# Performance work log

Hardware: AMD Instinct MI355X
Metric: run time of the kernel (lower is better)

The kernel has to match this reference:

```python
import jax, jax.numpy as jnp
import numpy as np

B, T, D, H1, H2, O = 64, 256, 512, 1024, 1024, 512


def setup_inputs() -> dict:
    key = jax.random.key(0)
    ks = jax.random.split(key, 6)
    s = 0.05  # weight scale for numerical sanity
    return {
        "x": jax.random.normal(ks[0], (B, T, D), dtype=jnp.float32),
        "W1": jax.random.normal(ks[1], (D, 4 * H1), dtype=jnp.float32) * s,
        "U1": jax.random.normal(ks[2], (H1, 4 * H1), dtype=jnp.float32) * s,
        "b1": jnp.zeros((4 * H1,), dtype=jnp.float32),
        "W2": jax.random.normal(ks[3], (H1, 4 * H2), dtype=jnp.float32) * s,
        "U2": jax.random.normal(ks[4], (H2, 4 * H2), dtype=jnp.float32) * s,
        "b2": jnp.zeros((4 * H2,), dtype=jnp.float32),
        "Wd": jax.random.normal(ks[5], (H2, O), dtype=jnp.float32) * s,
        "bd": jnp.zeros((O,), dtype=jnp.float32),
    }


def _lstm_layer(x_seq, W, U, b, units):
    """Run an LSTM layer over x_seq [B,T,Din]; returns full h sequence [B,T,units].

    Keras LSTMCell gate order: i, f, c(g), o; sigmoid recurrent activation, tanh activation.
    """
    # Precompute input projections for all timesteps: [T, B, 4*units]
    xz = (jnp.einsum('btd,dk->tbk', x_seq, W) + b).astype(x_seq.dtype)
    bsz = x_seq.shape[0]
    h0 = jnp.zeros((bsz, units), dtype=x_seq.dtype)
    c0 = jnp.zeros((bsz, units), dtype=x_seq.dtype)

    def step(carry, xz_t):
        h, c = carry
        z = xz_t + h @ U
        zi, zf, zg, zo = jnp.split(z, 4, axis=-1)
        c_new = jax.nn.sigmoid(zf) * c + jax.nn.sigmoid(zi) * jnp.tanh(zg)
        h_new = jax.nn.sigmoid(zo) * jnp.tanh(c_new)
        return (h_new, c_new), h_new

    (_, _), hs = jax.lax.scan(step, (h0, c0), xz)  # hs: [T, B, units]
    return jnp.transpose(hs, (1, 0, 2))


def reference(x, W1, U1, b1, W2, U2, b2, Wd, bd):
    seq1 = _lstm_layer(x, W1, U1, b1, H1)          # [B, T, H1]
    seq2 = _lstm_layer(seq1, W2, U2, b2, H2)       # [B, T, H2]
    h_last = seq2[:, -1, :]                        # final hidden state of layer 2
    return h_last @ Wd + bd
```

## Files before the change

### kernel.cpp

```cpp
#include <hip/hip_runtime.h>


typedef __bf16 bf16x8 __attribute__((ext_vector_type(8)));
typedef float f32x4 __attribute__((ext_vector_type(4)));
typedef unsigned int u32x4 __attribute__((ext_vector_type(4)));
typedef unsigned short u16;

#define LDS_Z_OFF 131584
#define LDS_TOTAL 148992

__device__ __forceinline__ u16 f2bf(float f) {
  unsigned u = __float_as_uint(f);
  unsigned r = (u + 0x7FFFu + ((u >> 16) & 1u)) >> 16;
  return (u16)r;
}

__global__ __launch_bounds__(256) void transpose_to_bf16(
    const float* __restrict__ in, u16* __restrict__ out, int R, int C) {
  __shared__ float tile[32][33];
  int tx = threadIdx.x & 31, ty = threadIdx.x >> 5;
  int c0 = blockIdx.x * 32, r0 = blockIdx.y * 32;
#pragma unroll
  for (int i = 0; i < 4; ++i)
    tile[ty + i * 8][tx] = in[(size_t)(r0 + ty + i * 8) * C + (c0 + tx)];
  __syncthreads();
#pragma unroll
  for (int i = 0; i < 4; ++i)
    out[(size_t)(c0 + ty + i * 8) * R + (r0 + tx)] = f2bf(tile[tx][ty + i * 8]);
}

__global__ __launch_bounds__(256) void convert_to_bf16(
    const float* __restrict__ in, u16* __restrict__ out, int n4) {
  int i = blockIdx.x * 256 + threadIdx.x;
  if (i >= n4) return;
  float4 v = reinterpret_cast<const float4*>(in)[i];
  ushort4 o;
  o.x = f2bf(v.x); o.y = f2bf(v.y); o.z = f2bf(v.z); o.w = f2bf(v.w);
  reinterpret_cast<ushort4*>(out)[i] = o;
}

__global__ void init_bar(unsigned* __restrict__ bar) { bar[threadIdx.x] = 0u; }

__device__ __forceinline__ void store_h_sc1(u16* p, unsigned v) {
  asm volatile("global_store_short %0, %1, off sc1" :: "v"(p), "v"(v) : "memory");
}

template <int I, int C0, int DEPTH, bool SC0, bool SC1>
__device__ __forceinline__ void stg_issue(u32x4 (&ring)[DEPTH],
    const u16* b0, const u16* b1) {
  constexpr int OFF = (I < C0 ? I : I - C0) * 256;
  if constexpr (I < C0) {
    if constexpr (SC0)
      asm volatile("global_load_dwordx4 %0, %1, off offset:%2 sc1"
                   : "=v"(ring[I % DEPTH]) : "v"(b0), "i"(OFF));
    else
      asm volatile("global_load_dwordx4 %0, %1, off offset:%2"
                   : "=v"(ring[I % DEPTH]) : "v"(b0), "i"(OFF));
  } else {
    if constexpr (SC1)
      asm volatile("global_load_dwordx4 %0, %1, off offset:%2 sc1"
                   : "=v"(ring[I % DEPTH]) : "v"(b1), "i"(OFF));
    else
      asm volatile("global_load_dwordx4 %0, %1, off offset:%2"
                   : "=v"(ring[I % DEPTH]) : "v"(b1), "i"(OFF));
  }
}

template <int I, int NPRE, int C0, int DEPTH, bool SC0, bool SC1>
__device__ __forceinline__ void stg_pre(u32x4 (&ring)[DEPTH],
    const u16* b0, const u16* b1) {
  if constexpr (I < NPRE) {
    stg_issue<I, C0, DEPTH, SC0, SC1>(ring, b0, b1);
    stg_pre<I + 1, NPRE, C0, DEPTH, SC0, SC1>(ring, b0, b1);
  }
}

template <int I, int NC, int C0, int DEPTH, bool SC0, bool SC1>
__device__ __forceinline__ void stg_main(u32x4 (&ring)[DEPTH],
    const u16* b0, const u16* b1, u16* lrow) {
  if constexpr (I < NC) {
    constexpr int ISSUED = (I + DEPTH < NC) ? I + DEPTH : NC;
    constexpr int WAIT = ISSUED - I - 1;
    asm volatile("s_waitcnt vmcnt(%1)" : "+v"(ring[I % DEPTH]) : "i"(WAIT));
    *(u32x4*)(lrow + I * 128) = ring[I % DEPTH];
    if constexpr (I + DEPTH < NC)
      stg_issue<I + DEPTH, C0, DEPTH, SC0, SC1>(ring, b0, b1);
    stg_main<I + 1, NC, C0, DEPTH, SC0, SC1>(ring, b0, b1, lrow);
  }
}

template <int NC, int C0, bool SC0, bool SC1>
__device__ __forceinline__ void stage(const u16* b0, const u16* b1, u16* lrow) {
  u32x4 ring[8];
  stg_pre<0, (NC < 8 ? NC : 8), C0, 8, SC0, SC1>(ring, b0, b1);
  stg_main<0, NC, C0, 8, SC0, SC1>(ring, b0, b1, lrow);
}

__device__ __forceinline__ void grid_barrier(unsigned* __restrict__ bar,
                                             int g, unsigned want) {
  asm volatile("s_waitcnt vmcnt(0)" ::: "memory");
  __syncthreads();
  if (threadIdx.x == 0) {
    unsigned old = __hip_atomic_fetch_add(bar + 32 * (1 + g), 1u,
                                          __ATOMIC_RELAXED, __HIP_MEMORY_SCOPE_AGENT);
    if (old == 32u * want - 1u) {
      unsigned r = __hip_atomic_fetch_add(bar, 1u, __ATOMIC_RELAXED,
                                          __HIP_MEMORY_SCOPE_AGENT);
      if (r == 8u * want - 1u) {
#pragma unroll
        for (int i = 0; i < 8; ++i)
          __hip_atomic_store(bar + 32 * (9 + i), want, __ATOMIC_RELAXED,
                             __HIP_MEMORY_SCOPE_AGENT);
      }
    }
    while (__hip_atomic_load(bar + 32 * (9 + g), __ATOMIC_RELAXED,
                             __HIP_MEMORY_SCOPE_AGENT) < want)
      __builtin_amdgcn_s_sleep(1);
  }
  __syncthreads();
}

template <int NC, int C0, bool SC0, bool IS2>
__device__ __forceinline__ void run_layer(
    const u16* __restrict__ xbf, const u16* __restrict__ Wt,
    const u16* __restrict__ Ut, const float* __restrict__ bias,
    u16* __restrict__ h1r, u16* __restrict__ h2r, unsigned* __restrict__ bar,
    int strip, int mhalf, char* smem, int g) {
  constexpr int KE = NC * 128;
  constexpr int P = KE + 8;
  constexpr int WCH = C0 * 4;
  u16* Alds = (u16*)smem;
  float* Zlds = (float*)(smem + LDS_Z_OFF);
  const int tid = threadIdx.x;
  const int wave = tid >> 6, lane = tid & 63;
  const int cp = wave & 1, kq = wave >> 1;
  const int quad = lane >> 4, l16 = lane & 15;

  bf16x8 breg[2][NC];
#pragma unroll
  for (int gi = 0; gi < 2; ++gi) {
    const int col = (2 * cp + gi) * 1024 + strip * 16 + l16;
#pragma unroll
    for (int j = 0; j < NC; ++j) {
      const int ks = kq * NC + j;
      breg[gi][j] = (ks < WCH)
        ? *(const bf16x8*)(Wt + (size_t)col * (C0 * 128) + ks * 32 + quad * 8)
        : *(const bf16x8*)(Ut + (size_t)col * 1024 + (ks - WCH) * 32 + quad * 8);
    }
  }

  const int eu = tid & 15, em = tid >> 4;
  const float bz0 = bias[strip * 16 + eu];
  const float bz1 = bias[1024 + strip * 16 + eu];
  const float bz2 = bias[2048 + strip * 16 + eu];
  const float bz3 = bias[3072 + strip * 16 + eu];
  float c = 0.f;

  const int sr = tid >> 4, l8 = tid & 15;
  const int sb = mhalf * 32 + sr;
  u16* lrow = Alds + sr * P + l8 * 8;

  const u16* a0p = Alds + l16 * P + quad * 8 + kq * (NC * 32);
  const u16* a1p = a0p + 16 * P;

  const int zc0 = cp * 32 + l16, zc1 = zc0 + 16;
  float* zb = Zlds + (kq & 1) * (32 * 68);

  for (int s = 0; s <= 256; ++s) {
    const int t = IS2 ? (s - 1) : s;
    if (t >= 0 && t < 256) {
      const u16 *b0, *b1;
      if constexpr (IS2) {
        b0 = h1r + (size_t)(t & 1) * 65536 + (size_t)sb * 1024 + l8 * 8;
        b1 = h2r + (size_t)((t - 1) & 1) * 65536 + (size_t)sb * 1024 + l8 * 8;
      } else {
        b0 = xbf + ((size_t)sb * 256 + t) * 512 + l8 * 8;
        b1 = h1r + (size_t)((t - 1) & 1) * 65536 + (size_t)sb * 1024 + l8 * 8;
      }
      if (t > 0) {
        stage<NC, C0, SC0, true>(b0, b1, lrow);
      } else {
        stage<C0, C0, SC0, true>(b0, b0, lrow);
#pragma unroll
        for (int i = C0; i < NC; ++i)
          *(u32x4*)(lrow + i * 128) = (u32x4){0u, 0u, 0u, 0u};
      }
      __syncthreads();

      f32x4 acc00 = {0.f, 0.f, 0.f, 0.f}, acc10 = {0.f, 0.f, 0.f, 0.f};
      f32x4 acc01 = {0.f, 0.f, 0.f, 0.f}, acc11 = {0.f, 0.f, 0.f, 0.f};
#pragma unroll
      for (int j = 0; j < NC; ++j) {
        bf16x8 a0 = *(const bf16x8*)(a0p + j * 32);
        bf16x8 a1 = *(const bf16x8*)(a1p + j * 32);
        acc00 = __builtin_amdgcn_mfma_f32_16x16x32_bf16(a0, breg[0][j], acc00, 0, 0, 0);
        acc10 = __builtin_amdgcn_mfma_f32_16x16x32_bf16(a1, breg[0][j], acc10, 0, 0, 0);
        acc01 = __builtin_amdgcn_mfma_f32_16x16x32_bf16(a0, breg[1][j], acc01, 0, 0, 0);
        acc11 = __builtin_amdgcn_mfma_f32_16x16x32_bf16(a1, breg[1][j], acc11, 0, 0, 0);
      }

      if (kq < 2) {
#pragma unroll
        for (int i = 0; i < 4; ++i) {
          zb[(quad * 4 + i) * 68 + zc0] = acc00[i];
          zb[(16 + quad * 4 + i) * 68 + zc0] = acc10[i];
          zb[(quad * 4 + i) * 68 + zc1] = acc01[i];
          zb[(16 + quad * 4 + i) * 68 + zc1] = acc11[i];
        }
      }
      __syncthreads();
      if (kq >= 2) {
#pragma unroll
        for (int i = 0; i < 4; ++i) {
          zb[(quad * 4 + i) * 68 + zc0] += acc00[i];
          zb[(16 + quad * 4 + i) * 68 + zc0] += acc10[i];
          zb[(quad * 4 + i) * 68 + zc1] += acc01[i];
          zb[(16 + quad * 4 + i) * 68 + zc1] += acc11[i];
        }
      }
      __syncthreads();

      u16* hring = IS2 ? h2r : h1r;
      u16* hp = hring + (size_t)(t & 1) * 65536 +
                (size_t)(mhalf * 32 + em) * 1024 + strip * 16 + eu;
      {
        float zi = Zlds[em * 68 + eu]      + Zlds[(32 + em) * 68 + eu]      + bz0;
        float zf = Zlds[em * 68 + 16 + eu] + Zlds[(32 + em) * 68 + 16 + eu] + bz1;
        float zg = Zlds[em * 68 + 32 + eu] + Zlds[(32 + em) * 68 + 32 + eu] + bz2;
        float zo = Zlds[em * 68 + 48 + eu] + Zlds[(32 + em) * 68 + 48 + eu] + bz3;
        float ig = 1.f / (1.f + __expf(-zi));
        float fg = 1.f / (1.f + __expf(-zf));
        float gg = 1.f - 2.f / (1.f + __expf(2.f * zg));
        float og = 1.f / (1.f + __expf(-zo));
        c = fg * c + ig * gg;
        float h = og * (1.f - 2.f / (1.f + __expf(2.f * c)));
        store_h_sc1(hp, (unsigned)f2bf(h));
      }
    }
    if (s < 256) grid_barrier(bar, g, (unsigned)(s + 1));
  }
}

__global__ __launch_bounds__(512, 2) void lstm_persistent(
    const u16* __restrict__ xbf,
    const u16* __restrict__ W1t,
    const u16* __restrict__ U1t,
    const float* __restrict__ b1,
    const u16* __restrict__ W2t,
    const u16* __restrict__ U2t,
    const float* __restrict__ b2,
    u16* __restrict__ h1r,
    u16* __restrict__ h2r,
    unsigned* __restrict__ bar) {
  extern __shared__ __align__(16) char smem[];
  const int blk = blockIdx.x;
  const bool is2 = blk >= 128;
  const int lb = is2 ? blk - 128 : blk;
  const int strip = lb >> 1;
  const int mhalf = lb & 1;
  const int g = blk & 7;
  if (!is2)
    run_layer<12, 4, false, false>(xbf, W1t, U1t, b1, h1r, h2r, bar,
                                   strip, mhalf, smem, g);
  else
    run_layer<16, 8, true, true>(xbf, W2t, U2t, b2, h1r, h2r, bar,
                                 strip, mhalf, smem, g);
}

__global__ __launch_bounds__(64) void dense_kernel(
    const u16* __restrict__ h2,
    const u16* __restrict__ Wdt,
    const float* __restrict__ bd,
    float* __restrict__ out) {
  int mt = blockIdx.x >> 5;
  int nt = blockIdx.x & 31;
  int lane = threadIdx.x;
  int quad = lane >> 4, l16 = lane & 15;
  f32x4 acc = {0.f, 0.f, 0.f, 0.f};
  const u16* ap = h2 + (size_t)(mt * 16 + l16) * 1024 + quad * 8;
  const u16* bp = Wdt + (size_t)(nt * 16 + l16) * 1024 + quad * 8;
#pragma unroll
  for (int ks = 0; ks < 32; ++ks) {
    bf16x8 a = *reinterpret_cast<const bf16x8*>(ap + ks * 32);
    bf16x8 b = *reinterpret_cast<const bf16x8*>(bp + ks * 32);
    acc = __builtin_amdgcn_mfma_f32_16x16x32_bf16(a, b, acc, 0, 0, 0);
  }
  int colo = nt * 16 + l16;
  float bias = bd[colo];
#pragma unroll
  for (int i = 0; i < 4; ++i)
    out[(size_t)(mt * 16 + quad * 4 + i) * 512 + colo] = acc[i] + bias;
}

extern "C" void kernel_launch(void* const* d_in, const int* in_sizes, int n_in,
                              void* d_out, int out_size, void* d_ws, size_t ws_size,
                              hipStream_t stream) {
  const float* x  = (const float*)d_in[0];
  const float* W1 = (const float*)d_in[1];
  const float* U1 = (const float*)d_in[2];
  const float* b1 = (const float*)d_in[3];
  const float* W2 = (const float*)d_in[4];
  const float* U2 = (const float*)d_in[5];
  const float* b2 = (const float*)d_in[6];
  const float* Wd = (const float*)d_in[7];
  const float* bd = (const float*)d_in[8];
  float* out = (float*)d_out;

  char* p = (char*)d_ws;
  auto carve = [&](size_t bytes) -> char* {
    char* r = p;
    p += (bytes + 255) & ~(size_t)255;
    return r;
  };
  u16* W1t = (u16*)carve((size_t)4096 * 512 * 2);
  u16* U1t = (u16*)carve((size_t)4096 * 1024 * 2);
  u16* W2t = (u16*)carve((size_t)4096 * 1024 * 2);
  u16* U2t = (u16*)carve((size_t)4096 * 1024 * 2);
  u16* Wdt = (u16*)carve((size_t)512 * 1024 * 2);
  u16* xbf = (u16*)carve((size_t)64 * 256 * 512 * 2);
  u16* h1r = (u16*)carve((size_t)2 * 64 * 1024 * 2);
  u16* h2r = (u16*)carve((size_t)2 * 64 * 1024 * 2);
  unsigned* bar = (unsigned*)carve(1024 * 4);
  (void)ws_size; (void)in_sizes; (void)n_in; (void)out_size;

  transpose_to_bf16<<<dim3(128, 16), 256, 0, stream>>>(W1, W1t, 512, 4096);
  transpose_to_bf16<<<dim3(128, 32), 256, 0, stream>>>(U1, U1t, 1024, 4096);
  transpose_to_bf16<<<dim3(128, 32), 256, 0, stream>>>(W2, W2t, 1024, 4096);
  transpose_to_bf16<<<dim3(128, 32), 256, 0, stream>>>(U2, U2t, 1024, 4096);
  transpose_to_bf16<<<dim3(16, 32), 256, 0, stream>>>(Wd, Wdt, 1024, 512);
  convert_to_bf16<<<8192, 256, 0, stream>>>(x, xbf, 64 * 256 * 512 / 4);
  init_bar<<<1, 1024, 0, stream>>>(bar);

  hipFuncSetAttribute(reinterpret_cast<const void*>(lstm_persistent),
                      hipFuncAttributeMaxDynamicSharedMemorySize, LDS_TOTAL);
  lstm_persistent<<<256, 512, LDS_TOTAL, stream>>>(
      xbf, W1t, U1t, b1, W2t, U2t, b2, h1r, h2r, bar);

  dense_kernel<<<128, 64, 0, stream>>>(h2r + 65536, Wdt, bd, out);
}
```

Baseline: 1.468 ms.

## Decouple LSTM layers with per-layer barriers and epoch flags over an 8-deep h1 ring

Replaces the single grid-wide barrier that locked both layers into one step with a separate 128-block barrier per layer. Layer 1 publishes an epoch counter after each step, and layer 2 polls it before consuming h1. Layer 1 in turn waits on layer 2's epoch so it never runs more than 8 steps ahead, and h1 moves to an 8-slot ring. This lets the layers drift relative to each other and shrinks each barrier, at the cost of extra polling and a larger h1 buffer.

```diff
diff --git a/kernel.cpp b/kernel.cpp
--- a/kernel.cpp
+++ b/kernel.cpp
@@ -39,7 +39,9 @@
   reinterpret_cast<ushort4*>(out)[i] = o;
 }
 
-__global__ void init_bar(unsigned* __restrict__ bar) { bar[threadIdx.x] = 0u; }
+__global__ void init_bar(unsigned* __restrict__ bar) {
+  bar[blockIdx.x * 1024 + threadIdx.x] = 0u;
+}
 
 __device__ __forceinline__ void store_h_sc1(u16* p, unsigned v) {
   asm volatile("global_store_short %0, %1, off sc1" :: "v"(p), "v"(v) : "memory");
@@ -96,26 +98,40 @@
   stg_main<0, NC, C0, 8, SC0, SC1>(ring, b0, b1, lrow);
 }
 
-__device__ __forceinline__ void grid_barrier(unsigned* __restrict__ bar,
-                                             int g, unsigned want) {
+__device__ __forceinline__ void group_barrier(unsigned* __restrict__ ubar,
+                                              unsigned* __restrict__ epub,
+                                              int g, unsigned want) {
   asm volatile("s_waitcnt vmcnt(0)" ::: "memory");
   __syncthreads();
   if (threadIdx.x == 0) {
-    unsigned old = __hip_atomic_fetch_add(bar + 32 * (1 + g), 1u,
+    unsigned old = __hip_atomic_fetch_add(ubar + 32 * (1 + g), 1u,
                                           __ATOMIC_RELAXED, __HIP_MEMORY_SCOPE_AGENT);
     if (old == 32u * want - 1u) {
-      unsigned r = __hip_atomic_fetch_add(bar, 1u, __ATOMIC_RELAXED,
+      unsigned r = __hip_atomic_fetch_add(ubar, 1u, __ATOMIC_RELAXED,
                                           __HIP_MEMORY_SCOPE_AGENT);
-      if (r == 8u * want - 1u) {
-#pragma unroll
-        for (int i = 0; i < 8; ++i)
-          __hip_atomic_store(bar + 32 * (9 + i), want, __ATOMIC_RELAXED,
+      if (r == 4u * want - 1u) {
+        __hip_atomic_store(epub, want, __ATOMIC_RELAXED,
+                           __HIP_MEMORY_SCOPE_AGENT);
+#pragma unroll
+        for (int i = 0; i < 4; ++i)
+          __hip_atomic_store(ubar + 32 * (9 + i), want, __ATOMIC_RELAXED,
                              __HIP_MEMORY_SCOPE_AGENT);
       }
     }
-    while (__hip_atomic_load(bar + 32 * (9 + g), __ATOMIC_RELAXED,
+    while (__hip_atomic_load(ubar + 32 * (9 + g), __ATOMIC_RELAXED,
                              __HIP_MEMORY_SCOPE_AGENT) < want)
       __builtin_amdgcn_s_sleep(1);
+  }
+  __syncthreads();
+}
+
+__device__ __forceinline__ void wait_epoch(unsigned* __restrict__ p,
+                                           unsigned v, unsigned& seen) {
+  if (threadIdx.x == 0) {
+    while (seen < v) {
+      seen = __hip_atomic_load(p, __ATOMIC_RELAXED, __HIP_MEMORY_SCOPE_AGENT);
+      if (seen < v) __builtin_amdgcn_s_sleep(2);
+    }
   }
   __syncthreads();
 }
@@ -124,7 +140,9 @@
 __device__ __forceinline__ void run_layer(
     const u16* __restrict__ xbf, const u16* __restrict__ Wt,
     const u16* __restrict__ Ut, const float* __restrict__ bias,
-    u16* __restrict__ h1r, u16* __restrict__ h2r, unsigned* __restrict__ bar,
+    u16* __restrict__ h1r, u16* __restrict__ h2r,
+    unsigned* __restrict__ ubar, unsigned* __restrict__ epub,
+    unsigned* __restrict__ ewait,
     int strip, int mhalf, char* smem, int g) {
   constexpr int KE = NC * 128;
   constexpr int P = KE + 8;
@@ -166,78 +184,84 @@
   const int zc0 = cp * 32 + l16, zc1 = zc0 + 16;
   float* zb = Zlds + (kq & 1) * (32 * 68);
 
-  for (int s = 0; s <= 256; ++s) {
-    const int t = IS2 ? (s - 1) : s;
-    if (t >= 0 && t < 256) {
-      const u16 *b0, *b1;
-      if constexpr (IS2) {
-        b0 = h1r + (size_t)(t & 1) * 65536 + (size_t)sb * 1024 + l8 * 8;
-        b1 = h2r + (size_t)((t - 1) & 1) * 65536 + (size_t)sb * 1024 + l8 * 8;
-      } else {
-        b0 = xbf + ((size_t)sb * 256 + t) * 512 + l8 * 8;
-        b1 = h1r + (size_t)((t - 1) & 1) * 65536 + (size_t)sb * 1024 + l8 * 8;
+  unsigned eseen = 0;
+
+  for (int t = 0; t < 256; ++t) {
+    if constexpr (IS2) {
+      wait_epoch(ewait, (unsigned)(t + 1), eseen);
+    } else {
+      if (t >= 8) wait_epoch(ewait, (unsigned)(t - 7), eseen);
+    }
+
+    const u16 *b0, *b1;
+    if constexpr (IS2) {
+      b0 = h1r + (size_t)(t & 7) * 65536 + (size_t)sb * 1024 + l8 * 8;
+      b1 = h2r + (size_t)((t - 1) & 1) * 65536 + (size_t)sb * 1024 + l8 * 8;
+    } else {
+      b0 = xbf + ((size_t)sb * 256 + t) * 512 + l8 * 8;
+      b1 = h1r + (size_t)((t - 1) & 7) * 65536 + (size_t)sb * 1024 + l8 * 8;
+    }
+    if (t > 0) {
+      stage<NC, C0, SC0, true>(b0, b1, lrow);
+    } else {
+      stage<C0, C0, SC0, true>(b0, b0, lrow);
+#pragma unroll
+      for (int i = C0; i < NC; ++i)
+        *(u32x4*)(lrow + i * 128) = (u32x4){0u, 0u, 0u, 0u};
+    }
+    __syncthreads();
+
+    f32x4 acc00 = {0.f, 0.f, 0.f, 0.f}, acc10 = {0.f, 0.f, 0.f, 0.f};
+    f32x4 acc01 = {0.f, 0.f, 0.f, 0.f}, acc11 = {0.f, 0.f, 0.f, 0.f};
+#pragma unroll
+    for (int j = 0; j < NC; ++j) {
+      bf16x8 a0 = *(const bf16x8*)(a0p + j * 32);
+      bf16x8 a1 = *(const bf16x8*)(a1p + j * 32);
+      acc00 = __builtin_amdgcn_mfma_f32_16x16x32_bf16(a0, breg[0][j], acc00, 0, 0, 0);
+      acc10 = __builtin_amdgcn_mfma_f32_16x16x32_bf16(a1, breg[0][j], acc10, 0, 0, 0);
+      acc01 = __builtin_amdgcn_mfma_f32_16x16x32_bf16(a0, breg[1][j], acc01, 0, 0, 0);
+      acc11 = __builtin_amdgcn_mfma_f32_16x16x32_bf16(a1, breg[1][j], acc11, 0, 0, 0);
+    }
+
+    if (kq < 2) {
+#pragma unroll
+      for (int i = 0; i < 4; ++i) {
+        zb[(quad * 4 + i) * 68 + zc0] = acc00[i];
+        zb[(16 + quad * 4 + i) * 68 + zc0] = acc10[i];
+        zb[(quad * 4 + i) * 68 + zc1] = acc01[i];
+        zb[(16 + quad * 4 + i) * 68 + zc1] = acc11[i];
       }
-      if (t > 0) {
-        stage<NC, C0, SC0, true>(b0, b1, lrow);
-      } else {
-        stage<C0, C0, SC0, true>(b0, b0, lrow);
-#pragma unroll
-        for (int i = C0; i < NC; ++i)
-          *(u32x4*)(lrow + i * 128) = (u32x4){0u, 0u, 0u, 0u};
+    }
+    __syncthreads();
+    if (kq >= 2) {
+#pragma unroll
+      for (int i = 0; i < 4; ++i) {
+        zb[(quad * 4 + i) * 68 + zc0] += acc00[i];
+        zb[(16 + quad * 4 + i) * 68 + zc0] += acc10[i];
+        zb[(quad * 4 + i) * 68 + zc1] += acc01[i];
+        zb[(16 + quad * 4 + i) * 68 + zc1] += acc11[i];
       }
-      __syncthreads();
-
-      f32x4 acc00 = {0.f, 0.f, 0.f, 0.f}, acc10 = {0.f, 0.f, 0.f, 0.f};
-      f32x4 acc01 = {0.f, 0.f, 0.f, 0.f}, acc11 = {0.f, 0.f, 0.f, 0.f};
-#pragma unroll
-      for (int j = 0; j < NC; ++j) {
-        bf16x8 a0 = *(const bf16x8*)(a0p + j * 32);
-        bf16x8 a1 = *(const bf16x8*)(a1p + j * 32);
-        acc00 = __builtin_amdgcn_mfma_f32_16x16x32_bf16(a0, breg[0][j], acc00, 0, 0, 0);
-        acc10 = __builtin_amdgcn_mfma_f32_16x16x32_bf16(a1, breg[0][j], acc10, 0, 0, 0);
-        acc01 = __builtin_amdgcn_mfma_f32_16x16x32_bf16(a0, breg[1][j], acc01, 0, 0, 0);
-        acc11 = __builtin_amdgcn_mfma_f32_16x16x32_bf16(a1, breg[1][j], acc11, 0, 0, 0);
-      }
-
-      if (kq < 2) {
-#pragma unroll
-        for (int i = 0; i < 4; ++i) {
-          zb[(quad * 4 + i) * 68 + zc0] = acc00[i];
-          zb[(16 + quad * 4 + i) * 68 + zc0] = acc10[i];
-          zb[(quad * 4 + i) * 68 + zc1] = acc01[i];
-          zb[(16 + quad * 4 + i) * 68 + zc1] = acc11[i];
-        }
-      }
-      __syncthreads();
-      if (kq >= 2) {
-#pragma unroll
-        for (int i = 0; i < 4; ++i) {
-          zb[(quad * 4 + i) * 68 + zc0] += acc00[i];
-          zb[(16 + quad * 4 + i) * 68 + zc0] += acc10[i];
-          zb[(quad * 4 + i) * 68 + zc1] += acc01[i];
-          zb[(16 + quad * 4 + i) * 68 + zc1] += acc11[i];
-        }
-      }
-      __syncthreads();
-
-      u16* hring = IS2 ? h2r : h1r;
-      u16* hp = hring + (size_t)(t & 1) * 65536 +
-                (size_t)(mhalf * 32 + em) * 1024 + strip * 16 + eu;
-      {
-        float zi = Zlds[em * 68 + eu]      + Zlds[(32 + em) * 68 + eu]      + bz0;
-        float zf = Zlds[em * 68 + 16 + eu] + Zlds[(32 + em) * 68 + 16 + eu] + bz1;
-        float zg = Zlds[em * 68 + 32 + eu] + Zlds[(32 + em) * 68 + 32 + eu] + bz2;
-        float zo = Zlds[em * 68 + 48 + eu] + Zlds[(32 + em) * 68 + 48 + eu] + bz3;
-        float ig = 1.f / (1.f + __expf(-zi));
-        float fg = 1.f / (1.f + __expf(-zf));
-        float gg = 1.f - 2.f / (1.f + __expf(2.f * zg));
-        float og = 1.f / (1.f + __expf(-zo));
-        c = fg * c + ig * gg;
-        float h = og * (1.f - 2.f / (1.f + __expf(2.f * c)));
-        store_h_sc1(hp, (unsigned)f2bf(h));
-      }
-    }
-    if (s < 256) grid_barrier(bar, g, (unsigned)(s + 1));
+    }
+    __syncthreads();
+
+    u16* hp = IS2
+      ? h2r + (size_t)(t & 1) * 65536 + (size_t)(mhalf * 32 + em) * 1024 + strip * 16 + eu
+      : h1r + (size_t)(t & 7) * 65536 + (size_t)(mhalf * 32 + em) * 1024 + strip * 16 + eu;
+    {
+      float zi = Zlds[em * 68 + eu]      + Zlds[(32 + em) * 68 + eu]      + bz0;
+      float zf = Zlds[em * 68 + 16 + eu] + Zlds[(32 + em) * 68 + 16 + eu] + bz1;
+      float zg = Zlds[em * 68 + 32 + eu] + Zlds[(32 + em) * 68 + 32 + eu] + bz2;
+      float zo = Zlds[em * 68 + 48 + eu] + Zlds[(32 + em) * 68 + 48 + eu] + bz3;
+      float ig = 1.f / (1.f + __expf(-zi));
+      float fg = 1.f / (1.f + __expf(-zf));
+      float gg = 1.f - 2.f / (1.f + __expf(2.f * zg));
+      float og = 1.f / (1.f + __expf(-zo));
+      c = fg * c + ig * gg;
+      float h = og * (1.f - 2.f / (1.f + __expf(2.f * c)));
+      store_h_sc1(hp, (unsigned)f2bf(h));
+    }
+
+    group_barrier(ubar, epub, g, (unsigned)(t + 1));
   }
 }
 
@@ -258,13 +282,16 @@
   const int lb = is2 ? blk - 128 : blk;
   const int strip = lb >> 1;
   const int mhalf = lb & 1;
-  const int g = blk & 7;
+  const int g = lb & 3;
+  unsigned* ubar  = bar + (is2 ? 2048 : 0);
+  unsigned* epub  = ubar + 512;
+  unsigned* ewait = (is2 ? bar : bar + 2048) + 512;
   if (!is2)
-    run_layer<12, 4, false, false>(xbf, W1t, U1t, b1, h1r, h2r, bar,
-                                   strip, mhalf, smem, g);
+    run_layer<12, 4, false, false>(xbf, W1t, U1t, b1, h1r, h2r,
+                                   ubar, epub, ewait, strip, mhalf, smem, g);
   else
-    run_layer<16, 8, true, true>(xbf, W2t, U2t, b2, h1r, h2r, bar,
-                                 strip, mhalf, smem, g);
+    run_layer<16, 8, true, true>(xbf, W2t, U2t, b2, h1r, h2r,
+                                 ubar, epub, ewait, strip, mhalf, smem, g);
 }
 
 __global__ __launch_bounds__(64) void dense_kernel(
@@ -318,9 +345,9 @@
   u16* U2t = (u16*)carve((size_t)4096 * 1024 * 2);
   u16* Wdt = (u16*)carve((size_t)512 * 1024 * 2);
   u16* xbf = (u16*)carve((size_t)64 * 256 * 512 * 2);
-  u16* h1r = (u16*)carve((size_t)2 * 64 * 1024 * 2);
+  u16* h1r = (u16*)carve((size_t)8 * 64 * 1024 * 2);
   u16* h2r = (u16*)carve((size_t)2 * 64 * 1024 * 2);
-  unsigned* bar = (unsigned*)carve(1024 * 4);
+  unsigned* bar = (unsigned*)carve(4096 * 4);
   (void)ws_size; (void)in_sizes; (void)n_in; (void)out_size;
 
   transpose_to_bf16<<<dim3(128, 16), 256, 0, stream>>>(W1, W1t, 512, 4096);
@@ -329,7 +356,7 @@
   transpose_to_bf16<<<dim3(128, 32), 256, 0, stream>>>(U2, U2t, 1024, 4096);
   transpose_to_bf16<<<dim3(16, 32), 256, 0, stream>>>(Wd, Wdt, 1024, 512);
   convert_to_bf16<<<8192, 256, 0, stream>>>(x, xbf, 64 * 256 * 512 / 4);
-  init_bar<<<1, 1024, 0, stream>>>(bar);
+  init_bar<<<4, 1024, 0, stream>>>(bar);
 
   hipFuncSetAttribute(reinterpret_cast<const void*>(lstm_persistent),
                       hipFuncAttributeMaxDynamicSharedMemorySize, LDS_TOTAL);
```

Result: no change. 1.477 ms (+0.6%).
